# Kernel tuning notes

Measured on AMD Instinct MI355X. Metric: run time of the kernel, lower is better.

Reference implementation:

```python
import jax, jax.numpy as jnp
import numpy as np

EMBED_DIM = 768
NUM_HEADS = 12


def setup_inputs() -> dict:
    key = jax.random.key(0)
    ks = jax.random.split(key, 9)
    B, N, C = 16, 1024, EMBED_DIM
    std = 1.0 / np.sqrt(C)
    x = jax.random.normal(ks[0], (B, N, C), dtype=jnp.float32)
    def w(k):
        return jax.random.normal(k, (C, C), dtype=jnp.float32) * std
    def b(k):
        return jax.random.normal(k, (C,), dtype=jnp.float32) * 0.01
    return {
        "x": x,
        "Wq": w(ks[1]), "bq": b(ks[2]),
        "Wk": w(ks[3]), "bk": b(ks[4]),
        "Wv": w(ks[5]), "bv": b(ks[6]),
        "Wo": w(ks[7]), "bo": b(ks[8]),
    }


def reference(x, Wq, bq, Wk, bk, Wv, bv, Wo, bo):
    B, N, C = x.shape
    H = NUM_HEADS
    Dh = C // H
    scale = 1.0 / np.sqrt(Dh)

    q = x @ Wq + bq  # (B, N, C)
    k = x @ Wk + bk
    v = x @ Wv + bv

    # Faithful to the original: (B, N, H, Dh) -> reshape(B*H, N, Dh)
    # WITHOUT transposing, exactly as torch_mla_core does (row-major reshape).
    q2 = q.reshape(B * H, N, Dh)
    k2 = k.reshape(B * H, N, Dh)
    v2 = v.reshape(B * H, N, Dh)

    scores = jnp.einsum('gld,gmd->glm', q2, k2) * scale  # (B*H, N, N)
    attn = jax.nn.softmax(scores, axis=-1)
    ctx2 = jnp.einsum('glm,gmd->gld', attn, v2)  # (B*H, N, Dh)

    ctx = ctx2.reshape(B, H, N, Dh).transpose(0, 2, 1, 3).reshape(B, N, C)
    out = ctx @ Wo + bo
    return out
```

## Files before the change

kernel.cpp:

```cpp
#include <hip/hip_runtime.h>
#include <hip/hip_bf16.h>
#include <cstdint>
#include <cstddef>

typedef unsigned short u16;
typedef __attribute__((ext_vector_type(8))) short s8v;
typedef __attribute__((ext_vector_type(4))) float f4v;
typedef __attribute__((ext_vector_type(8))) u16 u16x8;
typedef __attribute__((ext_vector_type(4))) uint32_t u32x4;

#define AS1 __attribute__((address_space(1)))
#define AS3 __attribute__((address_space(3)))

#define BATCH 16
#define SEQ   1024
#define EMBED 768
#define HEADS 12
#define DH    64
#define MTOT  (BATCH*SEQ)

__device__ __forceinline__ u16 f2bf(float f) {
    union { float f; uint32_t u; } v; v.f = f;
    uint32_t r = v.u + 0x7fffu + ((v.u >> 16) & 1u);
    return (u16)(r >> 16);
}

__device__ __forceinline__ void gll16(const u16* g, u16* l) {
    __builtin_amdgcn_global_load_lds((AS1 void*)g, (AS3 void*)l, 16, 0, 0);
}

#define XBLOCKS 12288
__global__ void k_pack(const float* __restrict__ x, u16* __restrict__ xb, int nx,
                       const float* __restrict__ Wq, const float* __restrict__ Wk,
                       const float* __restrict__ Wv, const float* __restrict__ Wo,
                       const float* __restrict__ bq, const float* __restrict__ bk,
                       const float* __restrict__ bv,
                       u16* __restrict__ wqkvT, u16* __restrict__ woT,
                       float* __restrict__ bqkv)
{
    if (blockIdx.x < XBLOCKS) {
        int i = (blockIdx.x * 256 + threadIdx.x) * 4;
        if (i + 3 < nx) {
            float4 f = *(const float4*)(x + i);
            ushort4 o;
            o.x = f2bf(f.x); o.y = f2bf(f.y); o.z = f2bf(f.z); o.w = f2bf(f.w);
            *(ushort4*)(xb + i) = o;
        }
        return;
    }
    const int NQKV = 2304 * 768;
    const int NO = 768 * 768;
    int t = (blockIdx.x - XBLOCKS) * 256 + threadIdx.x;
    if (t < NQKV) {
        int n = t % 2304, k = t / 2304;
        const float* src; int nn; float sc;
        if (n < 768)       { src = Wq; nn = n;        sc = 0.125f; }
        else if (n < 1536) { src = Wk; nn = n - 768;  sc = 1.0f;   }
        else               { src = Wv; nn = n - 1536; sc = 1.0f;   }
        wqkvT[(size_t)n * 768 + k] = f2bf(src[(size_t)k * 768 + nn] * sc);
    } else if (t < NQKV + NO) {
        int t2 = t - NQKV;
        int n = t2 % 768, k = t2 / 768;
        woT[(size_t)n * 768 + k] = f2bf(Wo[(size_t)k * 768 + n]);
    } else if (t < NQKV + NO + 2304) {
        int t3 = t - NQKV - NO;
        bqkv[t3] = (t3 < 768) ? bq[t3] * 0.125f
                 : ((t3 < 1536) ? bk[t3 - 768] : bv[t3 - 1536]);
    }
}

#define NT 12

template<int MODE>
__global__ __launch_bounds__(512, 2) void k_gemm8(
    const u16* __restrict__ A, const u16* __restrict__ BT,
    const float* __restrict__ bias,
    u16* __restrict__ oq, u16* __restrict__ okk, u16* __restrict__ ov,
    float* __restrict__ of, int NBN)
{
    __shared__ __attribute__((aligned(16))) u16 AB[2][16384];
    __shared__ __attribute__((aligned(16))) u16 BB[2][16384];

    const int nwg = gridDim.x;
    const int bid = blockIdx.x;
    const int wg = (bid & 7) * (nwg >> 3) + (bid >> 3);
    const int bm = wg / NBN, bn = wg % NBN;
    const int m0 = bm * 256, n0 = bn * 256;

    const int tid = threadIdx.x, wv = tid >> 6;
    const int ln = tid & 63, l15 = ln & 15, quad = ln >> 4;
    const int wm = wv >> 2, wn = wv & 3;

    const int chnk = ((tid & 7) ^ ((tid >> 3) & 7)) * 8;
    const u16* pA = A + (size_t)(m0 + (tid >> 3)) * 768 + chnk;
    const u16* pB = BT + (size_t)(n0 + (tid >> 8) * 64 + ((tid >> 3) & 31)) * 768 + chnk;

#define STG_A(BUF, mh, kt) { \
    const u16* s_ = pA + (mh) * 49152 + (kt) * 64; \
    gll16(s_,          (BUF) + (mh) * 8192 + wv * 512); \
    gll16(s_ + 98304,  (BUF) + (mh) * 8192 + 4096 + wv * 512); }
#define STG_B(BUF, nh, kt) { \
    const u16* s_ = pB + (nh) * 24576 + (kt) * 64; \
    gll16(s_,          (BUF) + (nh) * 8192 + wv * 512); \
    gll16(s_ + 98304,  (BUF) + (nh) * 8192 + 4096 + wv * 512); }

    const int offA = wm * 4096 + l15 * 64;
    const int offB = wn * 2048 + l15 * 64;
    const int ph0 = ((quad)     ^ (l15 & 7)) * 8;
    const int ph1 = ((4 + quad) ^ (l15 & 7)) * 8;

    f4v acc[8][4] = {};

    STG_A(&AB[0][0], 0, 0); STG_B(&BB[0][0], 0, 0);
    STG_A(&AB[0][0], 1, 0); STG_B(&BB[0][0], 1, 0);
    STG_A(&AB[1][0], 0, 1); STG_B(&BB[1][0], 0, 1);

#define PHASE(mh, nh, STAGE) { \
    s8v a_[4][2], b_[2][2]; \
    _Pragma("unroll") \
    for (int i = 0; i < 4; ++i) { \
        a_[i][0] = *(const s8v*)(Acur + offA + (mh) * 8192 + i * 1024 + ph0); \
        a_[i][1] = *(const s8v*)(Acur + offA + (mh) * 8192 + i * 1024 + ph1); } \
    _Pragma("unroll") \
    for (int j = 0; j < 2; ++j) { \
        b_[j][0] = *(const s8v*)(Bcur + offB + (nh) * 8192 + j * 1024 + ph0); \
        b_[j][1] = *(const s8v*)(Bcur + offB + (nh) * 8192 + j * 1024 + ph1); } \
    STAGE; \
    __builtin_amdgcn_s_barrier(); \
    __builtin_amdgcn_s_setprio(1); \
    _Pragma("unroll") \
    for (int i = 0; i < 4; ++i) \
    _Pragma("unroll") \
    for (int j = 0; j < 2; ++j) { \
        acc[(mh)*4+i][(nh)*2+j] = __builtin_amdgcn_mfma_f32_16x16x32_bf16(a_[i][0], b_[j][0], acc[(mh)*4+i][(nh)*2+j], 0, 0, 0); \
        acc[(mh)*4+i][(nh)*2+j] = __builtin_amdgcn_mfma_f32_16x16x32_bf16(a_[i][1], b_[j][1], acc[(mh)*4+i][(nh)*2+j], 0, 0, 0); } \
    __builtin_amdgcn_s_setprio(0); \
    __builtin_amdgcn_s_barrier(); }

    for (int s = 0; s < NT; ++s) {
        const int cur = s & 1;
        u16* Acur = &AB[cur][0];
        u16* Bcur = &BB[cur][0];
        u16* Anxt = &AB[cur ^ 1][0];
        u16* Bnxt = &BB[cur ^ 1][0];

        if (s == NT - 1) { asm volatile("s_waitcnt vmcnt(0)" ::: "memory"); }
        else             { asm volatile("s_waitcnt vmcnt(4)" ::: "memory"); }
        __builtin_amdgcn_s_barrier();

        PHASE(0, 0, if (s < NT - 1) STG_A(Anxt, 1, s + 1));
        PHASE(0, 1, if (s < NT - 1) STG_B(Bnxt, 1, s + 1));
        PHASE(1, 0, if (s < NT - 2) STG_A(Acur, 0, s + 2));
        PHASE(1, 1, if (s < NT - 2) STG_B(Bcur, 0, s + 2));
    }
#undef PHASE
#undef STG_A
#undef STG_B

#pragma unroll
    for (int jg = 0; jg < 4; ++jg) {
        int n = n0 + wn * 64 + jg * 16 + l15;
        float bs = bias[n];
        if (MODE == 0) {
            u16* dst; int nn;
            if (n < 768)       { dst = oq;  nn = n; }
            else if (n < 1536) { dst = okk; nn = n - 768; }
            else               { dst = ov;  nn = n - 1536; }
#pragma unroll
            for (int ig = 0; ig < 8; ++ig) {
                int mrow = m0 + wm * 128 + ig * 16 + quad * 4;
#pragma unroll
                for (int rg = 0; rg < 4; ++rg)
                    dst[(size_t)(mrow + rg) * 768 + nn] = f2bf(acc[ig][jg][rg] + bs);
            }
        } else {
#pragma unroll
            for (int ig = 0; ig < 8; ++ig) {
                int mrow = m0 + wm * 128 + ig * 16 + quad * 4;
#pragma unroll
                for (int rg = 0; rg < 4; ++rg)
                    of[(size_t)(mrow + rg) * 768 + n] = acc[ig][jg][rg] + bs;
            }
        }
    }
}

__global__ void k_transpose_v(const u16* __restrict__ v, u16* __restrict__ vt) {
    __shared__ __attribute__((aligned(16))) u16 ts[64 * 80];
    int g = blockIdx.x >> 4;
    int l0 = (blockIdx.x & 15) << 6;
    const u16* vg = v + (size_t)g * 65536;
    u16* vtg = vt + (size_t)g * 65536;
    int tid = threadIdx.x;
#pragma unroll
    for (int c = tid; c < 512; c += 256) {
        int l = c >> 3, d0 = (c & 7) * 8;
        *(uint4*)(ts + l * 80 + d0) = *(const uint4*)(vg + (size_t)(l0 + l) * 64 + d0);
    }
    __syncthreads();
#pragma unroll
    for (int c = tid; c < 512; c += 256) {
        int d = c >> 3, lc = (c & 7) * 8;
        u16x8 tv;
#pragma unroll
        for (int i = 0; i < 8; ++i) tv[i] = ts[(lc + i) * 80 + d];
        *(u16x8*)(vtg + (size_t)d * 1024 + l0 + lc) = tv;
    }
}

#define KS2(r_, c_) ( ((r_) << 6) + (((((c_) >> 3) ^ ((r_) & 7)) & 7) << 3) + ((c_) & 7) )

__global__ __launch_bounds__(256) void k_attn(
    const u16* __restrict__ qb, const u16* __restrict__ kb,
    const u16* __restrict__ vt, u16* __restrict__ ctx)
{
    __shared__ __attribute__((aligned(16))) u16 Ks[128 * 64];
    __shared__ __attribute__((aligned(16))) u16 Vts[64 * 136];

    const int g = blockIdx.x >> 4;
    const int q0 = (blockIdx.x & 15) << 6;
    const int tid = threadIdx.x, wv = tid >> 6;
    const int ln = tid & 63, l15 = ln & 15, quad = ln >> 4;
    const u16* qg = qb + (size_t)g * 65536;
    const u16* kg = kb + (size_t)g * 65536;
    const u16* vtg = vt + (size_t)g * 65536;

    const u16* qrow = qg + (size_t)(q0 + wv * 16 + l15) * 64 + quad * 8;
    s8v aQ0 = *(const s8v*)qrow;
    s8v aQ1 = *(const s8v*)(qrow + 32);

    const int krr = tid >> 3, kcb = (tid & 7) * 8;
    const int vd = tid >> 4, vc0 = (tid & 15) * 8;
    const u16* kgp = kg + (size_t)krr * 64 + kcb;
    const u16* vgp = vtg + (size_t)vd * 1024 + vc0;

    f4v o[4] = {};
    float rsum = 0.f;

    for (int jt = 0; jt < 8; ++jt) {
        __syncthreads();
        {
            const size_t koff = (size_t)jt * 8192;
            const int voff = jt * 128;
            uint4 kv0 = *(const uint4*)(kgp + koff);
            uint4 kv1 = *(const uint4*)(kgp + koff + 2048);
            uint4 kv2 = *(const uint4*)(kgp + koff + 4096);
            uint4 kv3 = *(const uint4*)(kgp + koff + 6144);
            uint4 vv0 = *(const uint4*)(vgp + voff);
            uint4 vv1 = *(const uint4*)(vgp + voff + 16384);
            uint4 vv2 = *(const uint4*)(vgp + voff + 32768);
            uint4 vv3 = *(const uint4*)(vgp + voff + 49152);
            *(uint4*)(Ks + KS2(krr,      kcb)) = kv0;
            *(uint4*)(Ks + KS2(krr + 32, kcb)) = kv1;
            *(uint4*)(Ks + KS2(krr + 64, kcb)) = kv2;
            *(uint4*)(Ks + KS2(krr + 96, kcb)) = kv3;
            *(uint4*)(Vts + (vd     ) * 136 + vc0) = vv0;
            *(uint4*)(Vts + (vd + 16) * 136 + vc0) = vv1;
            *(uint4*)(Vts + (vd + 32) * 136 + vc0) = vv2;
            *(uint4*)(Vts + (vd + 48) * 136 + vc0) = vv3;
        }
        __syncthreads();

        f4v s[8];
        __builtin_amdgcn_s_setprio(1);
#pragma unroll
        for (int ns = 0; ns < 8; ++ns) {
            int rK = ns * 16 + l15;
            s8v b0 = *(const s8v*)(Ks + KS2(rK, quad * 8));
            s8v b1 = *(const s8v*)(Ks + KS2(rK, quad * 8 + 32));
            f4v t = {};
            t = __builtin_amdgcn_mfma_f32_16x16x32_bf16(b0, aQ0, t, 0, 0, 0);
            t = __builtin_amdgcn_mfma_f32_16x16x32_bf16(b1, aQ1, t, 0, 0, 0);
            s[ns] = t;
        }
        __builtin_amdgcn_s_setprio(0);

#pragma unroll
        for (int ns = 0; ns < 8; ++ns)
#pragma unroll
            for (int rg = 0; rg < 4; ++rg) {
                float p = __expf(s[ns][rg]);
                s[ns][rg] = p;
                rsum += p;
            }

        __builtin_amdgcn_s_setprio(1);
#pragma unroll
        for (int ks = 0; ks < 4; ++ks) {
            uint32_t a0, a1, c0, c1;
            asm("v_cvt_pk_bf16_f32 %0, %1, %2" : "=v"(a0) : "v"(s[2*ks][0]),   "v"(s[2*ks][1]));
            asm("v_cvt_pk_bf16_f32 %0, %1, %2" : "=v"(a1) : "v"(s[2*ks][2]),   "v"(s[2*ks][3]));
            asm("v_cvt_pk_bf16_f32 %0, %1, %2" : "=v"(c0) : "v"(s[2*ks+1][0]), "v"(s[2*ks+1][1]));
            asm("v_cvt_pk_bf16_f32 %0, %1, %2" : "=v"(c1) : "v"(s[2*ks+1][2]), "v"(s[2*ks+1][3]));
            asm("v_permlane32_swap_b32 %0, %1" : "+v"(a0), "+v"(c0));
            asm("v_permlane16_swap_b32 %0, %1" : "+v"(a0), "+v"(c0));
            asm("v_permlane32_swap_b32 %0, %1" : "+v"(a1), "+v"(c1));
            asm("v_permlane16_swap_b32 %0, %1" : "+v"(a1), "+v"(c1));
            u32x4 pk; pk.x = a0; pk.y = a1; pk.z = c0; pk.w = c1;
            s8v aP = __builtin_bit_cast(s8v, pk);
#pragma unroll
            for (int ds = 0; ds < 4; ++ds) {
                s8v bV = *(const s8v*)(Vts + (ds * 16 + l15) * 136 + ks * 32 + quad * 8);
                o[ds] = __builtin_amdgcn_mfma_f32_16x16x32_bf16(aP, bV, o[ds], 0, 0, 0);
            }
        }
        __builtin_amdgcn_s_setprio(0);
    }

    rsum += __shfl_xor(rsum, 16, 64);
    rsum += __shfl_xor(rsum, 32, 64);

    const int b = g / 12, h = g % 12;
    u16* cbase = ctx + (size_t)b * 786432 + h * 64;
#pragma unroll
    for (int rg = 0; rg < 4; ++rg) {
        float rs = __shfl(rsum, 20 * quad + rg, 64);
        float inv = 1.0f / rs;
        int row = q0 + wv * 16 + quad * 4 + rg;
#pragma unroll
        for (int ds = 0; ds < 4; ++ds)
            cbase[(size_t)row * 768 + ds * 16 + l15] = f2bf(o[ds][rg] * inv);
    }
}

extern "C" void kernel_launch(void* const* d_in, const int* in_sizes, int n_in,
                              void* d_out, int out_size, void* d_ws, size_t ws_size,
                              hipStream_t stream) {
    const float* x  = (const float*)d_in[0];
    const float* Wq = (const float*)d_in[1];
    const float* bq = (const float*)d_in[2];
    const float* Wk = (const float*)d_in[3];
    const float* bk = (const float*)d_in[4];
    const float* Wv = (const float*)d_in[5];
    const float* bv = (const float*)d_in[6];
    const float* Wo = (const float*)d_in[7];
    const float* bo = (const float*)d_in[8];
    float* out = (float*)d_out;

    const size_t NTOK = (size_t)MTOT * EMBED;
    char* w = (char*)d_ws;
    u16* xb    = (u16*)w;              w += NTOK * 2;
    u16* qb    = (u16*)w;              w += NTOK * 2;
    u16* kb    = (u16*)w;              w += NTOK * 2;
    u16* vb    = (u16*)w;              w += NTOK * 2;
    u16* vtb   = (u16*)w;              w += NTOK * 2;
    u16* wqkvT = (u16*)w;              w += (size_t)2304 * 768 * 2;
    u16* woT   = (u16*)w;              w += (size_t)768 * 768 * 2;
    float* bqkv = (float*)w;           w += 2304 * 4;
    u16* ctx = xb;

    k_pack<<<XBLOCKS + 9225, 256, 0, stream>>>(x, xb, (int)NTOK,
        Wq, Wk, Wv, Wo, bq, bk, bv, wqkvT, woT, bqkv);

    k_gemm8<0><<<576, 512, 0, stream>>>(xb, wqkvT, bqkv, qb, kb, vb, nullptr, 9);

    k_transpose_v<<<3072, 256, 0, stream>>>(vb, vtb);
    k_attn<<<3072, 256, 0, stream>>>(qb, kb, vtb, ctx);

    k_gemm8<1><<<192, 512, 0, stream>>>(ctx, woT, bo, nullptr, nullptr, nullptr, out, 3);
}
```

Baseline: 364.1 us.

## Reuse GEMM fragment registers across phases and prefetch attention K/V tiles

In the projection GEMM, the four phase macros are unrolled by hand so A and B fragments loaded from LDS are kept in registers and reused across phases. This roughly halves the LDS fragment reads per k-step, at the cost of more live registers. In the attention kernel, the next K/V tile is loaded from global memory into registers while the current tile is being computed, replacing the two __syncthreads with raw barriers plus an lgkmcnt wait. This hides global load latency behind compute, but adds 8 uint4 registers per thread and depends on explicit wait counts being correct.

```diff
diff --git a/kernel.cpp b/kernel.cpp
--- a/kernel.cpp
+++ b/kernel.cpp
@@ -110,32 +110,11 @@
     const int ph1 = ((4 + quad) ^ (l15 & 7)) * 8;
 
     f4v acc[8][4] = {};
+    s8v aR[4][2], bR0[2][2], bR1[2][2];
 
     STG_A(&AB[0][0], 0, 0); STG_B(&BB[0][0], 0, 0);
     STG_A(&AB[0][0], 1, 0); STG_B(&BB[0][0], 1, 0);
     STG_A(&AB[1][0], 0, 1); STG_B(&BB[1][0], 0, 1);
-
-#define PHASE(mh, nh, STAGE) { \
-    s8v a_[4][2], b_[2][2]; \
-    _Pragma("unroll") \
-    for (int i = 0; i < 4; ++i) { \
-        a_[i][0] = *(const s8v*)(Acur + offA + (mh) * 8192 + i * 1024 + ph0); \
-        a_[i][1] = *(const s8v*)(Acur + offA + (mh) * 8192 + i * 1024 + ph1); } \
-    _Pragma("unroll") \
-    for (int j = 0; j < 2; ++j) { \
-        b_[j][0] = *(const s8v*)(Bcur + offB + (nh) * 8192 + j * 1024 + ph0); \
-        b_[j][1] = *(const s8v*)(Bcur + offB + (nh) * 8192 + j * 1024 + ph1); } \
-    STAGE; \
-    __builtin_amdgcn_s_barrier(); \
-    __builtin_amdgcn_s_setprio(1); \
-    _Pragma("unroll") \
-    for (int i = 0; i < 4; ++i) \
-    _Pragma("unroll") \
-    for (int j = 0; j < 2; ++j) { \
-        acc[(mh)*4+i][(nh)*2+j] = __builtin_amdgcn_mfma_f32_16x16x32_bf16(a_[i][0], b_[j][0], acc[(mh)*4+i][(nh)*2+j], 0, 0, 0); \
-        acc[(mh)*4+i][(nh)*2+j] = __builtin_amdgcn_mfma_f32_16x16x32_bf16(a_[i][1], b_[j][1], acc[(mh)*4+i][(nh)*2+j], 0, 0, 0); } \
-    __builtin_amdgcn_s_setprio(0); \
-    __builtin_amdgcn_s_barrier(); }
 
     for (int s = 0; s < NT; ++s) {
         const int cur = s & 1;
@@ -148,12 +127,78 @@
         else             { asm volatile("s_waitcnt vmcnt(4)" ::: "memory"); }
         __builtin_amdgcn_s_barrier();
 
-        PHASE(0, 0, if (s < NT - 1) STG_A(Anxt, 1, s + 1));
-        PHASE(0, 1, if (s < NT - 1) STG_B(Bnxt, 1, s + 1));
-        PHASE(1, 0, if (s < NT - 2) STG_A(Acur, 0, s + 2));
-        PHASE(1, 1, if (s < NT - 2) STG_B(Bcur, 0, s + 2));
-    }
-#undef PHASE
+#pragma unroll
+        for (int i = 0; i < 4; ++i) {
+            aR[i][0] = *(const s8v*)(Acur + offA + i * 1024 + ph0);
+            aR[i][1] = *(const s8v*)(Acur + offA + i * 1024 + ph1);
+        }
+#pragma unroll
+        for (int j = 0; j < 2; ++j) {
+            bR0[j][0] = *(const s8v*)(Bcur + offB + j * 1024 + ph0);
+            bR0[j][1] = *(const s8v*)(Bcur + offB + j * 1024 + ph1);
+        }
+        if (s < NT - 1) STG_A(Anxt, 1, s + 1);
+        __builtin_amdgcn_s_barrier();
+        __builtin_amdgcn_s_setprio(1);
+#pragma unroll
+        for (int i = 0; i < 4; ++i)
+#pragma unroll
+            for (int j = 0; j < 2; ++j) {
+                acc[i][j] = __builtin_amdgcn_mfma_f32_16x16x32_bf16(aR[i][0], bR0[j][0], acc[i][j], 0, 0, 0);
+                acc[i][j] = __builtin_amdgcn_mfma_f32_16x16x32_bf16(aR[i][1], bR0[j][1], acc[i][j], 0, 0, 0);
+            }
+        __builtin_amdgcn_s_setprio(0);
+        __builtin_amdgcn_s_barrier();
+
+#pragma unroll
+        for (int j = 0; j < 2; ++j) {
+            bR1[j][0] = *(const s8v*)(Bcur + offB + 8192 + j * 1024 + ph0);
+            bR1[j][1] = *(const s8v*)(Bcur + offB + 8192 + j * 1024 + ph1);
+        }
+        if (s < NT - 1) STG_B(Bnxt, 1, s + 1);
+        __builtin_amdgcn_s_barrier();
+        __builtin_amdgcn_s_setprio(1);
+#pragma unroll
+        for (int i = 0; i < 4; ++i)
+#pragma unroll
+            for (int j = 0; j < 2; ++j) {
+                acc[i][2 + j] = __builtin_amdgcn_mfma_f32_16x16x32_bf16(aR[i][0], bR1[j][0], acc[i][2 + j], 0, 0, 0);
+                acc[i][2 + j] = __builtin_amdgcn_mfma_f32_16x16x32_bf16(aR[i][1], bR1[j][1], acc[i][2 + j], 0, 0, 0);
+            }
+        __builtin_amdgcn_s_setprio(0);
+        __builtin_amdgcn_s_barrier();
+
+#pragma unroll
+        for (int i = 0; i < 4; ++i) {
+            aR[i][0] = *(const s8v*)(Acur + offA + 8192 + i * 1024 + ph0);
+            aR[i][1] = *(const s8v*)(Acur + offA + 8192 + i * 1024 + ph1);
+        }
+        if (s < NT - 2) STG_A(Acur, 0, s + 2);
+        __builtin_amdgcn_s_barrier();
+        __builtin_amdgcn_s_setprio(1);
+#pragma unroll
+        for (int i = 0; i < 4; ++i)
+#pragma unroll
+            for (int j = 0; j < 2; ++j) {
+                acc[4 + i][j] = __builtin_amdgcn_mfma_f32_16x16x32_bf16(aR[i][0], bR0[j][0], acc[4 + i][j], 0, 0, 0);
+                acc[4 + i][j] = __builtin_amdgcn_mfma_f32_16x16x32_bf16(aR[i][1], bR0[j][1], acc[4 + i][j], 0, 0, 0);
+            }
+        __builtin_amdgcn_s_setprio(0);
+        __builtin_amdgcn_s_barrier();
+
+        if (s < NT - 2) STG_B(Bcur, 0, s + 2);
+        __builtin_amdgcn_s_barrier();
+        __builtin_amdgcn_s_setprio(1);
+#pragma unroll
+        for (int i = 0; i < 4; ++i)
+#pragma unroll
+            for (int j = 0; j < 2; ++j) {
+                acc[4 + i][2 + j] = __builtin_amdgcn_mfma_f32_16x16x32_bf16(aR[i][0], bR1[j][0], acc[4 + i][2 + j], 0, 0, 0);
+                acc[4 + i][2 + j] = __builtin_amdgcn_mfma_f32_16x16x32_bf16(aR[i][1], bR1[j][1], acc[4 + i][2 + j], 0, 0, 0);
+            }
+        __builtin_amdgcn_s_setprio(0);
+        __builtin_amdgcn_s_barrier();
+    }
 #undef STG_A
 #undef STG_B
 
@@ -225,41 +270,56 @@
     const u16* kg = kb + (size_t)g * 65536;
     const u16* vtg = vt + (size_t)g * 65536;
 
-    const u16* qrow = qg + (size_t)(q0 + wv * 16 + l15) * 64 + quad * 8;
-    s8v aQ0 = *(const s8v*)qrow;
-    s8v aQ1 = *(const s8v*)(qrow + 32);
-
     const int krr = tid >> 3, kcb = (tid & 7) * 8;
     const int vd = tid >> 4, vc0 = (tid & 15) * 8;
     const u16* kgp = kg + (size_t)krr * 64 + kcb;
     const u16* vgp = vtg + (size_t)vd * 1024 + vc0;
 
+    uint4 kr0 = *(const uint4*)(kgp);
+    uint4 kr1 = *(const uint4*)(kgp + 2048);
+    uint4 kr2 = *(const uint4*)(kgp + 4096);
+    uint4 kr3 = *(const uint4*)(kgp + 6144);
+    uint4 vr0 = *(const uint4*)(vgp);
+    uint4 vr1 = *(const uint4*)(vgp + 16384);
+    uint4 vr2 = *(const uint4*)(vgp + 32768);
+    uint4 vr3 = *(const uint4*)(vgp + 49152);
+
+    const u16* qrow = qg + (size_t)(q0 + wv * 16 + l15) * 64 + quad * 8;
+    s8v aQ0 = *(const s8v*)qrow;
+    s8v aQ1 = *(const s8v*)(qrow + 32);
+
     f4v o[4] = {};
     float rsum = 0.f;
 
     for (int jt = 0; jt < 8; ++jt) {
-        __syncthreads();
-        {
-            const size_t koff = (size_t)jt * 8192;
-            const int voff = jt * 128;
-            uint4 kv0 = *(const uint4*)(kgp + koff);
-            uint4 kv1 = *(const uint4*)(kgp + koff + 2048);
-            uint4 kv2 = *(const uint4*)(kgp + koff + 4096);
-            uint4 kv3 = *(const uint4*)(kgp + koff + 6144);
-            uint4 vv0 = *(const uint4*)(vgp + voff);
-            uint4 vv1 = *(const uint4*)(vgp + voff + 16384);
-            uint4 vv2 = *(const uint4*)(vgp + voff + 32768);
-            uint4 vv3 = *(const uint4*)(vgp + voff + 49152);
-            *(uint4*)(Ks + KS2(krr,      kcb)) = kv0;
-            *(uint4*)(Ks + KS2(krr + 32, kcb)) = kv1;
-            *(uint4*)(Ks + KS2(krr + 64, kcb)) = kv2;
-            *(uint4*)(Ks + KS2(krr + 96, kcb)) = kv3;
-            *(uint4*)(Vts + (vd     ) * 136 + vc0) = vv0;
-            *(uint4*)(Vts + (vd + 16) * 136 + vc0) = vv1;
-            *(uint4*)(Vts + (vd + 32) * 136 + vc0) = vv2;
-            *(uint4*)(Vts + (vd + 48) * 136 + vc0) = vv3;
-        }
-        __syncthreads();
+        __builtin_amdgcn_s_barrier();
+        __builtin_amdgcn_sched_barrier(0);
+
+        *(uint4*)(Ks + KS2(krr,      kcb)) = kr0;
+        *(uint4*)(Ks + KS2(krr + 32, kcb)) = kr1;
+        *(uint4*)(Ks + KS2(krr + 64, kcb)) = kr2;
+        *(uint4*)(Ks + KS2(krr + 96, kcb)) = kr3;
+        *(uint4*)(Vts + (vd     ) * 136 + vc0) = vr0;
+        *(uint4*)(Vts + (vd + 16) * 136 + vc0) = vr1;
+        *(uint4*)(Vts + (vd + 32) * 136 + vc0) = vr2;
+        *(uint4*)(Vts + (vd + 48) * 136 + vc0) = vr3;
+
+        if (jt < 7) {
+            const size_t koff = (size_t)(jt + 1) * 8192;
+            const int voff = (jt + 1) * 128;
+            kr0 = *(const uint4*)(kgp + koff);
+            kr1 = *(const uint4*)(kgp + koff + 2048);
+            kr2 = *(const uint4*)(kgp + koff + 4096);
+            kr3 = *(const uint4*)(kgp + koff + 6144);
+            vr0 = *(const uint4*)(vgp + voff);
+            vr1 = *(const uint4*)(vgp + voff + 16384);
+            vr2 = *(const uint4*)(vgp + voff + 32768);
+            vr3 = *(const uint4*)(vgp + voff + 49152);
+        }
+
+        asm volatile("s_waitcnt lgkmcnt(0)" ::: "memory");
+        __builtin_amdgcn_s_barrier();
+        __builtin_amdgcn_sched_barrier(0);
 
         f4v s[8];
         __builtin_amdgcn_s_setprio(1);
```

Result: faster. 332.7 us (-8.6%).
